# Performance work log

Hardware: AMD Instinct MI355X
Metric: run time of the kernel (lower is better)

The kernel has to match this reference:

```python
import math
import jax, jax.numpy as jnp
import numpy as np

B, N, D, H, PQ, PV = 2, 2048, 256, 8, 4, 8
HD = D // H
OUT_IN = D + H * PV * 3 + H  # 256 + 192 + 8 = 456


def setup_inputs() -> dict:
    key = jax.random.key(0)
    ks = jax.random.split(key, 12)
    w = lambda k, shape: (jax.random.normal(k, shape, jnp.float32) * 0.02)
    return {
        "x": jax.random.normal(ks[0], (B, N, D), jnp.float32),
        "rotations": jax.random.normal(ks[1], (B, N, 3, 3), jnp.float32),
        "translations": jax.random.normal(ks[2], (B, N, 3), jnp.float32),
        "mask": jnp.ones((B, N), dtype=bool),
        "Wq": w(ks[3], (D, D)), "bq": jnp.zeros((D,), jnp.float32),
        "Wk": w(ks[4], (D, D)), "bk": jnp.zeros((D,), jnp.float32),
        "Wv": w(ks[5], (D, D)), "bv": jnp.zeros((D,), jnp.float32),
        "Wo": w(ks[6], (OUT_IN, D)), "bo": jnp.zeros((D,), jnp.float32),
        "head_weights": jnp.ones((H,), jnp.float32),
    }


def reference(x, rotations, translations, mask, Wq, bq, Wk, bk, Wv, bv, Wo, bo, head_weights):
    b, n, d = x.shape
    h = head_weights.shape[0]
    hd = d // h
    pv3 = Wo.shape[0] - d - h  # num_heads * num_value_points * 3

    q = (x @ Wq + bq).reshape(b, n, h, hd)
    k = (x @ Wk + bk).reshape(b, n, h, hd)
    v = (x @ Wv + bv).reshape(b, n, h, hd)

    # scalar attention logits [b,h,i,j]
    attn_scores = jnp.einsum("bihd,bjhd->bhij", q, k) / math.sqrt(hd)

    # point-distance bias from frame translations (rotated q/k/v points are
    # dead code in the original module and are omitted)
    diff = translations[:, :, None, :] - translations[:, None, :, :]  # [b,i,j,3]
    dist_sq = jnp.sum(diff * diff, axis=-1)                            # [b,i,j]
    point_attn = -0.5 * dist_sq[:, None, :, :]                         # [b,1,i,j]

    weights = jax.nn.softmax(head_weights)                             # [h]
    combined = attn_scores + point_attn * weights[None, :, None, None]
    combined = jnp.where(mask[:, None, None, :], combined, -1e9)
    attn_probs = jax.nn.softmax(combined, axis=-1)                     # [b,h,i,j]

    attn_output = jnp.einsum("bhij,bjhd->bihd", attn_probs, v).reshape(b, n, d)

    # translation-weighted points, brought back to local frame
    trans_weighted = jnp.einsum("bhij,bjc->bihc", attn_probs, translations)  # [b,i,h,3]
    trans_local = trans_weighted - translations[:, :, None, :]
    point_out = trans_local.reshape(b, n, h * 3)
    point_out = jnp.pad(point_out, ((0, 0), (0, 0), (0, pv3 - h * 3)))

    mean_dist = jnp.sqrt(jnp.mean(dist_sq, axis=-1, keepdims=True) + 1e-8)  # [b,n,1]
    pair_features = jnp.broadcast_to(mean_dist, (b, n, h))

    output = jnp.concatenate([attn_output, point_out, pair_features], axis=-1)
    return output @ Wo + bo
```

## Files before the change

### kernel.cpp

```cpp
#include <hip/hip_runtime.h>

typedef unsigned short u16;
typedef __attribute__((ext_vector_type(8))) short bf16x8;
typedef __attribute__((ext_vector_type(4))) float f32x4;
typedef __attribute__((ext_vector_type(16))) float f32x16;
typedef __attribute__((ext_vector_type(4))) unsigned u32x4;

#define NB 2
#define NSEQ 2048
#define DD 256
#define NH 8
#define NTOK 4096
#define KF 288
#define KFP 296
#define NSPLIT 4
#define PS 36
#define TSTR 2048

#define L_V 1024
#define L_A 2048
#define L_U 3072
#define L_ZP 3328
#define L_STR 3344

#define SCL2E 0.25506973f
#define L2E 1.4426950408889634f

__device__ __forceinline__ u16 f2b(float f) {
  unsigned u = __builtin_bit_cast(unsigned, f);
  return (u16)((u + 0x7fffu + ((u >> 16) & 1u)) >> 16);
}

__device__ __forceinline__ unsigned cvt_pk_bf16(float lo, float hi) {
  unsigned r;
  asm("v_cvt_pk_bf16_f32 %0, %1, %2" : "=v"(r) : "v"(lo), "v"(hi));
  return r;
}

__device__ __forceinline__ void permlane32_swap(unsigned& a, unsigned& b) {
  asm volatile("v_permlane32_swap_b32 %0, %1" : "+v"(a), "+v"(b));
}

__device__ __forceinline__ f32x4 mfma16(bf16x8 a, bf16x8 b, f32x4 c) {
  return __builtin_amdgcn_mfma_f32_16x16x32_bf16(a, b, c, 0, 0, 0);
}
__device__ __forceinline__ f32x16 mfma32(bf16x8 a, bf16x8 b, f32x16 c) {
  return __builtin_amdgcn_mfma_f32_32x32x16_bf16(a, b, c, 0, 0, 0);
}

#define PB_XB 1024
#define PB_WT (PB_XB + 264)
#define PB_BS (PB_WT + 2)
#define PB_T4 (PB_BS + 16)
#define PB_UC (PB_T4 + 128)
#define PB_AC (PB_UC + 64)
#define PB_N  (PB_AC + 1)
__global__ __launch_bounds__(256) void prep(
    const float* __restrict__ x, const float* __restrict__ tr,
    const float* __restrict__ hw, const float* __restrict__ bq,
    const float* __restrict__ bk, const float* __restrict__ bv,
    const float* __restrict__ Wq, const float* __restrict__ Wk,
    const float* __restrict__ Wv, const float* __restrict__ Wo,
    u16* __restrict__ xb, u16* __restrict__ WqkvT, u16* __restrict__ WoPT,
    float4* __restrict__ t4, float4* __restrict__ bstat,
    u16* __restrict__ UC, u16* __restrict__ AC,
    float* __restrict__ b_all, float* __restrict__ wsoft) {
  __shared__ float lt[32][33];
  __shared__ float4 red[4];
  const int bid = blockIdx.x, t = threadIdx.x;
  if (bid < PB_XB) {
    const int i4 = bid * 256 + t;
    float4 v = *(const float4*)(x + (size_t)i4 * 4);
    ushort4 o;
    o.x = f2b(v.x); o.y = f2b(v.y); o.z = f2b(v.z); o.w = f2b(v.w);
    *(ushort4*)(xb + (size_t)i4 * 4) = o;
  } else if (bid < PB_WT) {
    const int bw = bid - PB_XB;
    const int r = t >> 3, c4 = (t & 7) * 4;
    if (bw < 192) {
      int mt = bw >> 3, kt = bw & 7;
      int m0 = mt * 32, k0 = kt * 32;
      const float* W = m0 < 256 ? Wq : (m0 < 512 ? Wk : Wv);
      const int mm = m0 & 255;
      float4 v = *(const float4*)(W + (size_t)(k0 + r) * 256 + mm + c4);
      lt[r][c4] = v.x; lt[r][c4 + 1] = v.y; lt[r][c4 + 2] = v.z; lt[r][c4 + 3] = v.w;
      __syncthreads();
      const float s = m0 < 256 ? SCL2E : 1.f;
      ushort4 o;
      o.x = f2b(lt[c4][r] * s); o.y = f2b(lt[c4 + 1][r] * s);
      o.z = f2b(lt[c4 + 2][r] * s); o.w = f2b(lt[c4 + 3][r] * s);
      *(ushort4*)(WqkvT + (size_t)(m0 + r) * 256 + k0 + c4) = o;
    } else {
      int q = bw - 192;
      int nt2 = q / 9, kt = q - nt2 * 9;
      int n0 = nt2 * 32, kk0 = kt * 32;
      int row = (kk0 + r) < 280 ? (kk0 + r) : (kk0 + r + 168);
      float4 v = *(const float4*)(Wo + (size_t)row * 256 + n0 + c4);
      lt[r][c4] = v.x; lt[r][c4 + 1] = v.y; lt[r][c4 + 2] = v.z; lt[r][c4 + 3] = v.w;
      __syncthreads();
      ushort4 o;
      o.x = f2b(lt[c4][r]); o.y = f2b(lt[c4 + 1][r]);
      o.z = f2b(lt[c4 + 2][r]); o.w = f2b(lt[c4 + 3][r]);
      *(ushort4*)(WoPT + (size_t)(n0 + r) * KF + kk0 + c4) = o;
    }
  } else if (bid < PB_BS) {
    const int b = bid - PB_WT;
    float sx = 0.f, sy = 0.f, sz = 0.f, s2 = 0.f;
    for (int j = t; j < NSEQ; j += 256) {
      float a = tr[(size_t)(b * NSEQ + j) * 3];
      float b2 = tr[(size_t)(b * NSEQ + j) * 3 + 1];
      float c = tr[(size_t)(b * NSEQ + j) * 3 + 2];
      sx += a; sy += b2; sz += c; s2 += a * a + b2 * b2 + c * c;
    }
#pragma unroll
    for (int off = 1; off < 64; off <<= 1) {
      sx += __shfl_xor(sx, off); sy += __shfl_xor(sy, off);
      sz += __shfl_xor(sz, off); s2 += __shfl_xor(s2, off);
    }
    if ((t & 63) == 0) red[t >> 6] = make_float4(sx, sy, sz, s2);
    __syncthreads();
    if (t == 0) {
      float4 a = red[0], b1 = red[1], c = red[2], d = red[3];
      bstat[b] = make_float4(a.x + b1.x + c.x + d.x, a.y + b1.y + c.y + d.y,
                             a.z + b1.z + c.z + d.z, a.w + b1.w + c.w + d.w);
    }
  } else if (bid < PB_T4) {
    const int j = (bid - PB_BS) * 256 + t;
    float a = tr[j * 3], b2 = tr[j * 3 + 1], c = tr[j * 3 + 2];
    t4[j] = make_float4(a, b2, c, a * a + b2 * b2 + c * c);
  } else if (bid < PB_UC) {
    const int id = (bid - PB_T4) * 256 + t;
    const int b = id >> 14, jt = (id >> 8) & 63, c = (id >> 3) & 31, e = id & 7;
    const int tok = b * NSEQ + jt * 32 + c;
    float v = 0.f;
    if (e < 3) v = tr[(size_t)tok * 3 + e];
    else if (e == 3) {
      float a = tr[(size_t)tok * 3], b2 = tr[(size_t)tok * 3 + 1],
            cz = tr[(size_t)tok * 3 + 2];
      v = a * a + b2 * b2 + cz * cz;
    } else if (e == 4) v = 1.f;
    UC[id] = f2b(v);
  } else if (bid < PB_AC) {
    const int id = (bid - PB_UC) * 256 + t;
    const int b = id >> 13, jt = (id >> 7) & 63, sub = (id >> 5) & 3,
              cch = (id >> 3) & 3, e = id & 7;
    const int j = jt * 32 + (sub >> 1) * 16 + (sub & 1) * 8 + e;
    float v = cch == 0 ? 1.f : tr[(size_t)(b * NSEQ + j) * 3 + cch - 1];
    AC[id] = f2b(v);
  } else {
    for (int i = t; i < 768; i += 256)
      b_all[i] = i < 256 ? bq[i] * SCL2E : i < 512 ? bk[i - 256] : bv[i - 512];
    if (t == 0) {
      float mx = hw[0];
      for (int i = 1; i < NH; i++) mx = fmaxf(mx, hw[i]);
      float e[NH], sum = 0.f;
      for (int i = 0; i < NH; i++) { e[i] = __expf(hw[i] - mx); sum += e[i]; }
      for (int i = 0; i < NH; i++) wsoft[i] = e[i] / sum;
    }
  }
}

template <int M, int K>
__global__ __launch_bounds__(256) void gemm_big(
    const u16* __restrict__ AT, const u16* __restrict__ BT,
    const float* __restrict__ bias, u16* __restrict__ out) {
  const int lane = threadIdx.x & 63, wv = threadIdx.x >> 6;
  const int il = lane & 15, g = lane >> 4;
  const int wm = wv >> 1, wn = wv & 1;
  const int mblk = blockIdx.y * 64 + wm * 32;
  const int nblk = blockIdx.x * 128 + wn * 64;
  f32x4 acc[2][4];
#pragma unroll
  for (int a = 0; a < 2; a++)
#pragma unroll
    for (int b = 0; b < 4; b++) acc[a][b] = (f32x4)(0.f);
  const u16* Abase = AT + (size_t)(mblk + il) * K + 8 * g;
  const u16* Bbase = BT + (size_t)(nblk + il) * K + 8 * g;
#pragma unroll
  for (int kk = 0; kk < K; kk += 32) {
    bf16x8 aF[2], bF[4];
#pragma unroll
    for (int mt = 0; mt < 2; mt++)
      aF[mt] = *(const bf16x8*)(Abase + (size_t)mt * 16 * K + kk);
#pragma unroll
    for (int nt = 0; nt < 4; nt++)
      bF[nt] = *(const bf16x8*)(Bbase + (size_t)nt * 16 * K + kk);
#pragma unroll
    for (int mt = 0; mt < 2; mt++)
#pragma unroll
      for (int nt = 0; nt < 4; nt++)
        acc[mt][nt] = mfma16(aF[mt], bF[nt], acc[mt][nt]);
  }
#pragma unroll
  for (int nt = 0; nt < 4; nt++) {
    const int n_g = nblk + nt * 16 + il;
#pragma unroll
    for (int mt = 0; mt < 2; mt++) {
      const int m0 = mblk + mt * 16 + 4 * g;
      f32x4 v = acc[mt][nt];
      const float4 bb = *(const float4*)(bias + m0);
      v[0] += bb.x; v[1] += bb.y; v[2] += bb.z; v[3] += bb.w;
      ushort4 u;
      u.x = f2b(v[0]); u.y = f2b(v[1]); u.z = f2b(v[2]); u.w = f2b(v[3]);
      *(ushort4*)(out + (size_t)n_g * M + m0) = u;
    }
  }
}

__global__ __launch_bounds__(256) void repack(
    const u16* __restrict__ QKV, u16* __restrict__ TLB) {
  __shared__ u16 ldsV[32][33];
  const int jt = blockIdx.x, h = blockIdx.y, b = blockIdx.z;
  const int t = threadIdx.x;
  u16* tile = TLB + ((size_t)((b * NH + h) * 64 + jt)) * TSTR;
  if (t < 128) {
    const int rr = t & 31, dd = t >> 5;
    const int tok = b * NSEQ + jt * 32 + rr;
    bf16x8 kv = *(const bf16x8*)(QKV + (size_t)tok * 768 + 256 + h * 32 + dd * 8);
    *(bf16x8*)(tile + (size_t)(dd * 32 + rr) * 8) = kv;
  } else {
    const int u = t - 128;
    const int rr = u & 31, dd = u >> 5;
    const int tok = b * NSEQ + jt * 32 + rr;
    bf16x8 vv = *(const bf16x8*)(QKV + (size_t)tok * 768 + 512 + h * 32 + dd * 8);
#pragma unroll
    for (int e = 0; e < 8; e++) ldsV[rr][dd * 8 + e] = (u16)vv[e];
  }
  __syncthreads();
  if (t >= 128) {
    const int u = t - 128;
    const int c2 = u & 31, sub = u >> 5;
    const int jb2 = (sub >> 1) * 16 + (sub & 1) * 8;
    u16 ov[8];
#pragma unroll
    for (int e = 0; e < 8; e++) ov[e] = ldsV[jb2 + e][c2];
    *(bf16x8*)(tile + 1024 + (size_t)u * 8) = *(bf16x8*)ov;
  }
}

__global__ __launch_bounds__(256, 4) void attn_kernel(
    const u16* __restrict__ QKV, const u16* __restrict__ TLB,
    const u16* __restrict__ UC, const u16* __restrict__ AC,
    const float4* __restrict__ t4, const float* __restrict__ wsoft,
    float* __restrict__ part) {
  __shared__ __align__(16) u16 lds[2 * L_STR];
  const int tid = threadIdx.x;
  const int lane = tid & 63, wv = tid >> 6;
  const int c = lane & 31, hi = lane >> 5;
  const int bid = blockIdx.x;
  const int idx = bid >> 3;
  const int c2 = (bid & 7) * 8 + (idx >> 4);
  const int bh = c2 >> 2, s = c2 & 3;
  const int b = bh >> 3, h = bh & 7;
  const int qb = (idx & 15) * 128 + wv * 32;
  const int iglob = b * NSEQ + qb + c;

  const u16* qptr = QKV + (size_t)iglob * 768 + h * 32 + 8 * hi;
  const bf16x8 qf0 = *(const bf16x8*)qptr;
  const bf16x8 qf1 = *(const bf16x8*)(qptr + 16);
  const float4 ti = t4[iglob];
  const float w = wsoft[h];
  const float WD = w * L2E, NH2 = -0.5f * WD;
  u32x4 vw = (u32x4)(0u);
  if (hi == 0) {
    vw[0] = cvt_pk_bf16(WD * ti.x, WD * ti.y);
    vw[1] = cvt_pk_bf16(WD * ti.z, NH2);
    vw[2] = cvt_pk_bf16(NH2 * ti.w, 0.f);
  }
  const bf16x8 vf = __builtin_bit_cast(bf16x8, vw);

  f32x16 o = (f32x16)(0.f), aacc = (f32x16)(0.f);
  const int jt0 = s * 16;
  const u16* tK = TLB + ((size_t)bh * 64 + jt0) * TSTR;
  const u16* tA = AC + ((size_t)b * 64 + jt0) * 128;
  const u16* tU = UC + ((size_t)b * 64 + jt0) * 256;
  const int fo = hi * 256 + c * 8;

  {
    unsigned* zz = (unsigned*)lds;
    for (int i = tid; i < 1296; i += 256) {
      int k = (i < 648) ? (L_A / 2 + i) : (L_STR / 2 + L_A / 2 + i - 648);
      zz[k] = 0;
    }
  }
  __syncthreads();
  bf16x8 gkv = *(const bf16x8*)(tK + (size_t)tid * 8);
  bf16x8 ga, gu;
  if (tid < 16) ga = *(const bf16x8*)(tA + tid * 8);
  else if (tid < 48) gu = *(const bf16x8*)(tU + (tid - 16) * 8);
  *(bf16x8*)(lds + tid * 8) = gkv;
  if (tid < 16) *(bf16x8*)(lds + L_A + (tid >> 2) * 256 + (tid & 3) * 8) = ga;
  else if (tid < 48) *(bf16x8*)(lds + L_U + (tid - 16) * 8) = gu;
  __syncthreads();

#pragma unroll 1
  for (int t = 0; t < 16; ++t) {
    if (t < 15) {
      gkv = *(const bf16x8*)(tK + (size_t)(t + 1) * TSTR + tid * 8);
      if (tid < 16) ga = *(const bf16x8*)(tA + (size_t)(t + 1) * 128 + tid * 8);
      else if (tid < 48)
        gu = *(const bf16x8*)(tU + (size_t)(t + 1) * 256 + (tid - 16) * 8);
    }
    const u16* L = lds + (t & 1) * L_STR;
    bf16x8 k0 = *(const bf16x8*)(L + fo);
    bf16x8 k1 = *(const bf16x8*)(L + 512 + fo);
    bf16x8 v0 = *(const bf16x8*)(L + L_V + fo);
    bf16x8 v1 = *(const bf16x8*)(L + L_V + 512 + fo);
    bf16x8 a0 = *(const bf16x8*)(L + L_A + fo);
    bf16x8 a1 = *(const bf16x8*)(L + L_A + 512 + fo);
    bf16x8 uf = *(const bf16x8*)(hi ? (L + L_ZP) : (L + L_U + c * 8));
    __builtin_amdgcn_s_setprio(1);
    f32x16 sa = mfma32(uf, vf, (f32x16)(0.f));
    sa = mfma32(k0, qf0, sa);
    sa = mfma32(k1, qf1, sa);
    float p[16];
#pragma unroll
    for (int r = 0; r < 16; r++) p[r] = exp2f(sa[r]);
    unsigned x0 = cvt_pk_bf16(p[0], p[1]), y0 = cvt_pk_bf16(p[4], p[5]);
    unsigned z0 = cvt_pk_bf16(p[2], p[3]), w0 = cvt_pk_bf16(p[6], p[7]);
    permlane32_swap(x0, y0);
    permlane32_swap(z0, w0);
    unsigned x1 = cvt_pk_bf16(p[8], p[9]), y1 = cvt_pk_bf16(p[12], p[13]);
    unsigned z1 = cvt_pk_bf16(p[10], p[11]), w1 = cvt_pk_bf16(p[14], p[15]);
    permlane32_swap(x1, y1);
    permlane32_swap(z1, w1);
    bf16x8 pa0 = __builtin_bit_cast(bf16x8, (u32x4){x0, z0, y0, w0});
    bf16x8 pa1 = __builtin_bit_cast(bf16x8, (u32x4){x1, z1, y1, w1});
    o = mfma32(pa0, v0, o);
    o = mfma32(pa1, v1, o);
    aacc = mfma32(pa0, a0, aacc);
    aacc = mfma32(pa1, a1, aacc);
    __builtin_amdgcn_s_setprio(0);
    if (t < 15) {
      u16* D = lds + ((t + 1) & 1) * L_STR;
      *(bf16x8*)(D + tid * 8) = gkv;
      if (tid < 16) *(bf16x8*)(D + L_A + (tid >> 2) * 256 + (tid & 3) * 8) = ga;
      else if (tid < 48) *(bf16x8*)(D + L_U + (tid - 16) * 8) = gu;
    }
    __syncthreads();
  }

  float* pbase = part + ((size_t)(s * 16 + bh) * NSEQ + qb) * PS;
#pragma unroll
  for (int r = 0; r < 16; r++) {
    const int irow = (r & 3) + 8 * (r >> 2) + 4 * hi;
    float* pr = pbase + (size_t)irow * PS;
    pr[c] = o[r];
    if (c < 4) pr[32 + c] = aacc[r];
  }
}

__global__ __launch_bounds__(256) void outk(
    const float* __restrict__ part, const u16* __restrict__ WoPT,
    const float* __restrict__ bo, const float4* __restrict__ t4,
    const float4* __restrict__ bstat, const float* __restrict__ tr,
    float* __restrict__ out) {
  __shared__ __align__(16) u16 feats[16][KFP];
  __shared__ float invl[16][8];
  const int t = threadIdx.x;
  const int tok0 = blockIdx.x * 16;
  const int b = tok0 >> 11;
  const int i0 = tok0 & 2047;
  const size_t SS = (size_t)16 * NSEQ * PS;
  if (t < 128) {
    const int r = t >> 3, hh = t & 7;
    const float* p = part + ((size_t)(b * 8 + hh) * NSEQ + i0 + r) * PS + 32;
    invl[r][hh] = 1.f / (p[0] + p[SS] + p[2 * SS] + p[3 * SS]);
  }
  __syncthreads();
#pragma unroll
  for (int ii = 0; ii < 16; ++ii) {
    const int id = t + 256 * ii;
    const int r = id >> 8, cc = id & 255;
    const float* p =
        part + ((size_t)(b * 8 + (cc >> 5)) * NSEQ + i0 + r) * PS + (cc & 31);
    float v = p[0] + p[SS] + p[2 * SS] + p[3 * SS];
    feats[r][cc] = f2b(v * invl[r][cc >> 5]);
  }
  for (int id = t; id < 384; id += 256) {
    const int r = id / 24, cc = id - r * 24;
    const int comp = cc % 3, hh = cc / 3;
    const float* p =
        part + ((size_t)(b * 8 + hh) * NSEQ + i0 + r) * PS + 33 + comp;
    float v = p[0] + p[SS] + p[2 * SS] + p[3 * SS];
    feats[r][256 + cc] =
        f2b(v * invl[r][hh] - tr[(size_t)(tok0 + r) * 3 + comp]);
  }
  if (t < 128) {
    const int r = t >> 3;
    float4 tt = t4[tok0 + r];
    float4 st = bstat[b];
    float sumd = (float)NSEQ * tt.w + st.w -
                 2.f * (tt.x * st.x + tt.y * st.y + tt.z * st.z);
    feats[r][280 + (t & 7)] = f2b(sqrtf(sumd * (1.f / (float)NSEQ) + 1e-8f));
  }
  __syncthreads();
  const int lane = t & 63, wv = t >> 6;
  const int il = lane & 15, g = lane >> 4;
  f32x4 acc[4];
#pragma unroll
  for (int mt = 0; mt < 4; mt++) acc[mt] = (f32x4)(0.f);
  const u16* Ab = WoPT + (size_t)(wv * 64 + il) * KF + 8 * g;
#pragma unroll
  for (int kk = 0; kk < KF; kk += 32) {
    bf16x8 bF = *(const bf16x8*)(&feats[il][kk + 8 * g]);
#pragma unroll
    for (int mt = 0; mt < 4; mt++) {
      bf16x8 aF = *(const bf16x8*)(Ab + (size_t)mt * 16 * KF + kk);
      acc[mt] = mfma16(aF, bF, acc[mt]);
    }
  }
  const int n_g = tok0 + il;
#pragma unroll
  for (int mt = 0; mt < 4; mt++) {
    const int m0 = wv * 64 + mt * 16 + 4 * g;
    f32x4 v = acc[mt];
    const float4 bb = *(const float4*)(bo + m0);
    v[0] += bb.x; v[1] += bb.y; v[2] += bb.z; v[3] += bb.w;
    *(float4*)(out + (size_t)n_g * DD + m0) = make_float4(v[0], v[1], v[2], v[3]);
  }
}

extern "C" void kernel_launch(void* const* d_in, const int* in_sizes, int n_in,
                              void* d_out, int out_size, void* d_ws, size_t ws_size,
                              hipStream_t stream) {
  (void)in_sizes; (void)n_in; (void)out_size; (void)ws_size;
  const float* x  = (const float*)d_in[0];
  const float* tr = (const float*)d_in[2];
  const float* Wq = (const float*)d_in[4];
  const float* bq = (const float*)d_in[5];
  const float* Wk = (const float*)d_in[6];
  const float* bk = (const float*)d_in[7];
  const float* Wv = (const float*)d_in[8];
  const float* bv = (const float*)d_in[9];
  const float* Wo = (const float*)d_in[10];
  const float* bo = (const float*)d_in[11];
  const float* hw = (const float*)d_in[12];
  float* out = (float*)d_out;

  char* p = (char*)d_ws;
  auto alloc = [&](size_t n) { char* r = p; p += (n + 255) & ~(size_t)255; return r; };
  u16* xb      = (u16*)alloc((size_t)NTOK * DD * 2);
  u16* WqkvT   = (u16*)alloc((size_t)768 * DD * 2);
  u16* WoPT    = (u16*)alloc((size_t)DD * KF * 2);
  float4* t4   = (float4*)alloc((size_t)NTOK * 16);
  float* b_all = (float*)alloc(768 * 4);
  float* ws    = (float*)alloc(256);
  float4* bst  = (float4*)alloc(256);
  u16* UC      = (u16*)alloc((size_t)NB * 64 * 256 * 2);
  u16* AC      = (u16*)alloc((size_t)NB * 64 * 128 * 2);
  u16* QKV     = (u16*)alloc((size_t)NTOK * 768 * 2);
  u16* TLB     = (u16*)alloc((size_t)NB * NH * 64 * TSTR * 2);
  float* part  = (float*)alloc((size_t)NSPLIT * 16 * NSEQ * PS * 4);

  prep<<<PB_N, 256, 0, stream>>>(x, tr, hw, bq, bk, bv, Wq, Wk, Wv, Wo, xb,
                                 WqkvT, WoPT, t4, bst, UC, AC, b_all, ws);
  gemm_big<768, DD><<<dim3(32, 12), 256, 0, stream>>>(WqkvT, xb, b_all, QKV);
  repack<<<dim3(64, NH, NB), 256, 0, stream>>>(QKV, TLB);
  attn_kernel<<<1024, 256, 0, stream>>>(QKV, TLB, UC, AC, t4, ws, part);
  outk<<<256, 256, 0, stream>>>(part, WoPT, bo, t4, bst, tr, out);
}
```

Baseline: 138.8 us.

## Fuse K/V tile repacking into QKV GEMM epilogue and vectorize partial reduction

The QKV projection GEMM now writes Q to a compact buffer and scatters K and V straight into the attention tile layout, transposing V through shared memory in the epilogue. This removes the separate repack kernel launch and the round trip of K/V through global memory. The output kernel's reduction over split partials also switches to float4 loads. The cost is a more complex GEMM epilogue with an extra barrier and scattered stores for the V blocks.

Measured after the change: 138.9 us. About the same (+0.1%).

```diff
diff --git a/kernel.cpp b/kernel.cpp
--- a/kernel.cpp
+++ b/kernel.cpp
@@ -160,31 +160,33 @@
   }
 }
 
-template <int M, int K>
-__global__ __launch_bounds__(256) void gemm_big(
+__global__ __launch_bounds__(256) void gemm_qkv(
     const u16* __restrict__ AT, const u16* __restrict__ BT,
-    const float* __restrict__ bias, u16* __restrict__ out) {
+    const float* __restrict__ bias, u16* __restrict__ Qb,
+    u16* __restrict__ TLB) {
+  __shared__ u16 vt[128][65];
   const int lane = threadIdx.x & 63, wv = threadIdx.x >> 6;
   const int il = lane & 15, g = lane >> 4;
   const int wm = wv >> 1, wn = wv & 1;
-  const int mblk = blockIdx.y * 64 + wm * 32;
+  const int yb = blockIdx.y;
+  const int mblk = yb * 64 + wm * 32;
   const int nblk = blockIdx.x * 128 + wn * 64;
   f32x4 acc[2][4];
 #pragma unroll
   for (int a = 0; a < 2; a++)
 #pragma unroll
     for (int b = 0; b < 4; b++) acc[a][b] = (f32x4)(0.f);
-  const u16* Abase = AT + (size_t)(mblk + il) * K + 8 * g;
-  const u16* Bbase = BT + (size_t)(nblk + il) * K + 8 * g;
-#pragma unroll
-  for (int kk = 0; kk < K; kk += 32) {
+  const u16* Abase = AT + (size_t)(mblk + il) * DD + 8 * g;
+  const u16* Bbase = BT + (size_t)(nblk + il) * DD + 8 * g;
+#pragma unroll
+  for (int kk = 0; kk < DD; kk += 32) {
     bf16x8 aF[2], bF[4];
 #pragma unroll
     for (int mt = 0; mt < 2; mt++)
-      aF[mt] = *(const bf16x8*)(Abase + (size_t)mt * 16 * K + kk);
+      aF[mt] = *(const bf16x8*)(Abase + (size_t)mt * 16 * DD + kk);
 #pragma unroll
     for (int nt = 0; nt < 4; nt++)
-      bF[nt] = *(const bf16x8*)(Bbase + (size_t)nt * 16 * K + kk);
+      bF[nt] = *(const bf16x8*)(Bbase + (size_t)nt * 16 * DD + kk);
 #pragma unroll
     for (int mt = 0; mt < 2; mt++)
 #pragma unroll
@@ -202,44 +204,46 @@
       v[0] += bb.x; v[1] += bb.y; v[2] += bb.z; v[3] += bb.w;
       ushort4 u;
       u.x = f2b(v[0]); u.y = f2b(v[1]); u.z = f2b(v[2]); u.w = f2b(v[3]);
-      *(ushort4*)(out + (size_t)n_g * M + m0) = u;
-    }
-  }
-}
-
-__global__ __launch_bounds__(256) void repack(
-    const u16* __restrict__ QKV, u16* __restrict__ TLB) {
-  __shared__ u16 ldsV[32][33];
-  const int jt = blockIdx.x, h = blockIdx.y, b = blockIdx.z;
-  const int t = threadIdx.x;
-  u16* tile = TLB + ((size_t)((b * NH + h) * 64 + jt)) * TSTR;
-  if (t < 128) {
-    const int rr = t & 31, dd = t >> 5;
-    const int tok = b * NSEQ + jt * 32 + rr;
-    bf16x8 kv = *(const bf16x8*)(QKV + (size_t)tok * 768 + 256 + h * 32 + dd * 8);
-    *(bf16x8*)(tile + (size_t)(dd * 32 + rr) * 8) = kv;
-  } else {
-    const int u = t - 128;
-    const int rr = u & 31, dd = u >> 5;
-    const int tok = b * NSEQ + jt * 32 + rr;
-    bf16x8 vv = *(const bf16x8*)(QKV + (size_t)tok * 768 + 512 + h * 32 + dd * 8);
-#pragma unroll
-    for (int e = 0; e < 8; e++) ldsV[rr][dd * 8 + e] = (u16)vv[e];
-  }
-  __syncthreads();
-  if (t >= 128) {
-    const int u = t - 128;
-    const int c2 = u & 31, sub = u >> 5;
-    const int jb2 = (sub >> 1) * 16 + (sub & 1) * 8;
-    u16 ov[8];
-#pragma unroll
-    for (int e = 0; e < 8; e++) ov[e] = ldsV[jb2 + e][c2];
-    *(bf16x8*)(tile + 1024 + (size_t)u * 8) = *(bf16x8*)ov;
+      if (yb < 4) {
+        *(ushort4*)(Qb + (size_t)n_g * 256 + m0) = u;
+      } else if (yb < 8) {
+        const int f = m0 - 256;
+        const int h = f >> 5, dd = (f & 31) >> 3, e0 = f & 7;
+        const int b = n_g >> 11, jj = n_g & 2047;
+        const int jt = jj >> 5, c = jj & 31;
+        u16* tile = TLB + ((size_t)((b * NH + h) * 64 + jt)) * TSTR;
+        *(ushort4*)(tile + (size_t)(dd * 32 + c) * 8 + e0) = u;
+      } else {
+        const int ml = m0 - yb * 64;
+        const int nl = wn * 64 + nt * 16 + il;
+        vt[nl][ml] = u.x; vt[nl][ml + 1] = u.y;
+        vt[nl][ml + 2] = u.z; vt[nl][ml + 3] = u.w;
+      }
+    }
+  }
+  if (yb >= 8) {
+    __syncthreads();
+#pragma unroll
+    for (int ii = 0; ii < 4; ++ii) {
+      const int q = threadIdx.x + 256 * ii;
+      const int jt_loc = q >> 8, qq = q & 255;
+      const int sub = qq >> 6, h_loc = (qq >> 5) & 1, c = qq & 31;
+      const int jjb = (sub >> 1) * 16 + (sub & 1) * 8;
+      const int row0 = jt_loc * 32 + jjb;
+      u16 ov[8];
+#pragma unroll
+      for (int e = 0; e < 8; e++) ov[e] = vt[row0 + e][h_loc * 32 + c];
+      const int tok = blockIdx.x * 128 + row0;
+      const int b = tok >> 11, jj = tok & 2047, jt = jj >> 5;
+      const int h = (yb - 8) * 2 + h_loc;
+      u16* tile = TLB + ((size_t)((b * NH + h) * 64 + jt)) * TSTR + L_V;
+      *(bf16x8*)(tile + sub * 256 + c * 8) = *(bf16x8*)ov;
+    }
   }
 }
 
 __global__ __launch_bounds__(256, 4) void attn_kernel(
-    const u16* __restrict__ QKV, const u16* __restrict__ TLB,
+    const u16* __restrict__ Qb, const u16* __restrict__ TLB,
     const u16* __restrict__ UC, const u16* __restrict__ AC,
     const float4* __restrict__ t4, const float* __restrict__ wsoft,
     float* __restrict__ part) {
@@ -255,7 +259,7 @@
   const int qb = (idx & 15) * 128 + wv * 32;
   const int iglob = b * NSEQ + qb + c;
 
-  const u16* qptr = QKV + (size_t)iglob * 768 + h * 32 + 8 * hi;
+  const u16* qptr = Qb + (size_t)iglob * 256 + h * 32 + 8 * hi;
   const bf16x8 qf0 = *(const bf16x8*)qptr;
   const bf16x8 qf1 = *(const bf16x8*)(qptr + 16);
   const float4 ti = t4[iglob];
@@ -369,13 +373,23 @@
   }
   __syncthreads();
 #pragma unroll
-  for (int ii = 0; ii < 16; ++ii) {
+  for (int ii = 0; ii < 4; ++ii) {
     const int id = t + 256 * ii;
-    const int r = id >> 8, cc = id & 255;
+    const int r = id >> 6, q4 = id & 63;
+    const int cc = q4 * 4, hh = q4 >> 3;
     const float* p =
-        part + ((size_t)(b * 8 + (cc >> 5)) * NSEQ + i0 + r) * PS + (cc & 31);
-    float v = p[0] + p[SS] + p[2 * SS] + p[3 * SS];
-    feats[r][cc] = f2b(v * invl[r][cc >> 5]);
+        part + ((size_t)(b * 8 + hh) * NSEQ + i0 + r) * PS + (cc & 31);
+    float4 v0 = *(const float4*)p;
+    float4 v1 = *(const float4*)(p + SS);
+    float4 v2 = *(const float4*)(p + 2 * SS);
+    float4 v3 = *(const float4*)(p + 3 * SS);
+    const float inv = invl[r][hh];
+    ushort4 u;
+    u.x = f2b((v0.x + v1.x + v2.x + v3.x) * inv);
+    u.y = f2b((v0.y + v1.y + v2.y + v3.y) * inv);
+    u.z = f2b((v0.z + v1.z + v2.z + v3.z) * inv);
+    u.w = f2b((v0.w + v1.w + v2.w + v3.w) * inv);
+    *(ushort4*)(&feats[r][cc]) = u;
   }
   for (int id = t; id < 384; id += 256) {
     const int r = id / 24, cc = id - r * 24;
@@ -449,14 +463,13 @@
   float4* bst  = (float4*)alloc(256);
   u16* UC      = (u16*)alloc((size_t)NB * 64 * 256 * 2);
   u16* AC      = (u16*)alloc((size_t)NB * 64 * 128 * 2);
-  u16* QKV     = (u16*)alloc((size_t)NTOK * 768 * 2);
+  u16* Qb      = (u16*)alloc((size_t)NTOK * DD * 2);
   u16* TLB     = (u16*)alloc((size_t)NB * NH * 64 * TSTR * 2);
   float* part  = (float*)alloc((size_t)NSPLIT * 16 * NSEQ * PS * 4);
 
   prep<<<PB_N, 256, 0, stream>>>(x, tr, hw, bq, bk, bv, Wq, Wk, Wv, Wo, xb,
                                  WqkvT, WoPT, t4, bst, UC, AC, b_all, ws);
-  gemm_big<768, DD><<<dim3(32, 12), 256, 0, stream>>>(WqkvT, xb, b_all, QKV);
-  repack<<<dim3(64, NH, NB), 256, 0, stream>>>(QKV, TLB);
-  attn_kernel<<<1024, 256, 0, stream>>>(QKV, TLB, UC, AC, t4, ws, part);
+  gemm_qkv<<<dim3(32, 12), 256, 0, stream>>>(WqkvT, xb, b_all, Qb, TLB);
+  attn_kernel<<<1024, 256, 0, stream>>>(Qb, TLB, UC, AC, t4, ws, part);
   outk<<<256, 256, 0, stream>>>(part, WoPT, bo, t4, bst, tr, out);
 }
```
